# Kernel optimization log

Hardware: AMD Instinct MI355X
Metric: run time of the kernel (lower is better)

## Reference

```python
import jax, jax.numpy as jnp
import numpy as np

L_Q, B, Q = 512, 256, 512
IN, H, A = 512, 1024, 512
L_H = 512


def _xavier(key, shape):
    fan_out, fan_in = shape
    lim = (6.0 / (fan_in + fan_out)) ** 0.5
    return jax.random.uniform(key, shape, minval=-lim, maxval=lim, dtype=jnp.float32)


def setup_inputs() -> dict:
    key = jax.random.key(0)
    ks = jax.random.split(key, 12)
    return {
        "query_data": jax.random.normal(ks[0], (L_Q, B, Q), dtype=jnp.float32),
        "query_mask": jnp.ones((L_Q, B), dtype=jnp.float32),
        "input": jax.random.normal(ks[1], (B, IN), dtype=jnp.float32),
        "parent_index": jax.random.randint(ks[2], (B,), 0, L_H),
        "history": jax.random.normal(ks[3], (L_H, B, H), dtype=jnp.float32),
        "h0": jax.random.normal(ks[4], (B, H), dtype=jnp.float32),
        "c0": jax.random.normal(ks[5], (B, H), dtype=jnp.float32),
        "W_ih": _xavier(ks[6], (4 * H, IN + Q + H)),
        "W_hh": _xavier(ks[7], (4 * H, H)),
        "b_ih": jnp.zeros((4 * H,), dtype=jnp.float32),
        "b_hh": jnp.zeros((4 * H,), dtype=jnp.float32),
        "att1_w": _xavier(ks[8], (A, Q + H)),
        "att1_b": jnp.zeros((A,), dtype=jnp.float32),
        "att2_w": _xavier(ks[9], (1, A)),
        "att2_b": jnp.zeros((1,), dtype=jnp.float32),
    }


def reference(query_data, query_mask, input, parent_index, history, h0, c0,
              W_ih, W_hh, b_ih, b_hh, att1_w, att1_b, att2_w, att2_b):
    L_q, Bn, _ = query_data.shape
    # attention: concat broadcast h0 with query, two linears + tanh
    h_ctx = jnp.broadcast_to(h0[None], (L_q, Bn, h0.shape[1]))
    att = jnp.concatenate([h_ctx, query_data], axis=2)          # (L_q, B, H+Q)
    att_hidden = jnp.tanh(att @ att1_w.T + att1_b)               # (L_q, B, A)
    att_raw = (att_hidden @ att2_w.T + att2_b)[..., 0]           # (L_q, B)
    # manual masked softmax over L_q (faithful: max taken before masking)
    e = jnp.exp(att_raw - jnp.max(att_raw, axis=0, keepdims=True)) * query_mask
    w = e / jnp.sum(e, axis=0, keepdims=True)                    # (L_q, B)
    ctx_vec = jnp.sum(query_data * w[..., None], axis=0)         # (B, Q)
    # query_history: gather instead of one-hot matmul
    h_parent = history[parent_index, jnp.arange(Bn)]             # (B, H)
    # LSTMCell (dropout=0 -> identity); torch gate order i, f, g, o
    x = jnp.concatenate([input, ctx_vec, h_parent], axis=1)      # (B, IN+Q+H)
    gates = x @ W_ih.T + b_ih + h0 @ W_hh.T + b_hh               # (B, 4H)
    i, f, g, o = jnp.split(gates, 4, axis=1)
    c1 = jax.nn.sigmoid(f) * c0 + jax.nn.sigmoid(i) * jnp.tanh(g)
    h1 = jax.nn.sigmoid(o) * jnp.tanh(c1)
    return ctx_vec, h1, c1
```

## Files before the change

### kernel.cpp

```cpp
#include <hip/hip_runtime.h>
#include <hip/hip_bf16.h>


typedef short bf16x8 __attribute__((ext_vector_type(8)));
typedef float f32x4 __attribute__((ext_vector_type(4)));
typedef unsigned short u16x4 __attribute__((ext_vector_type(4)));

__device__ __forceinline__ unsigned short f2bf(float f) {
  unsigned int u = __builtin_bit_cast(unsigned int, f);
  u += 0x7fffu + ((u >> 16) & 1u);
  return (unsigned short)(u >> 16);
}
__device__ __forceinline__ float bf2f(unsigned short u) {
  unsigned int x = (unsigned int)u << 16;
  return __builtin_bit_cast(float, x);
}
__device__ __forceinline__ float fast_tanh(float x) {
  float e = __expf(2.0f * x);
  return 1.0f - 2.0f / (e + 1.0f);
}
__device__ __forceinline__ float fast_sig(float x) {
  return 1.0f / (1.0f + __expf(-x));
}
__device__ __forceinline__ f32x4 mfma16(bf16x8 a, bf16x8 b, f32x4 c) {
  return __builtin_amdgcn_mfma_f32_16x16x32_bf16(a, b, c, 0, 0, 0);
}

__global__ void k_prep(const float* __restrict__ a1w, const float* __restrict__ h0,
                       unsigned short* __restrict__ wqf, float* __restrict__ part1) {
  __shared__ float sh[4096], swt[4096];
  int bx = blockIdx.x;
  if (bx < 128) {
    int g = bx * 256 + threadIdx.x;
    int lane = g & 63, frag = g >> 6;
    int ab = frag >> 4, ksf = frag & 15;
    int a = ab * 16 + (lane & 15);
    int k = ksf * 32 + (lane >> 4) * 8;
    const float* src = a1w + (size_t)a * 1536 + 1024 + k;
    float4 v0 = *reinterpret_cast<const float4*>(src);
    float4 v1 = *reinterpret_cast<const float4*>(src + 4);
    unsigned short* dst = wqf + ((size_t)frag * 64 + lane) * 8;
    *(u16x4*)dst       = u16x4{ f2bf(v0.x), f2bf(v0.y), f2bf(v0.z), f2bf(v0.w) };
    *(u16x4*)(dst + 4) = u16x4{ f2bf(v1.x), f2bf(v1.y), f2bf(v1.z), f2bf(v1.w) };
    return;
  }
  int blk = bx - 128;
  int at = blk & 7, bt = (blk >> 3) & 3, ksp = blk >> 5;
  int a0 = at * 64, b0 = bt * 64, kbase = ksp * 128;
  int t = threadIdx.x;
  int ta = t & 15, tb = t >> 4;
  float acc[4][4] = {};
  for (int half = 0; half < 2; half++) {
    int k0 = kbase + half * 64;
    for (int i = 0; i < 4; i++) {
      int u = i * 256 + t;
      int row = u >> 4, c4 = (u & 15) << 2;
      float4 vh = *reinterpret_cast<const float4*>(h0 + (size_t)(b0 + row) * 1024 + k0 + c4);
      float4 vw = *reinterpret_cast<const float4*>(a1w + (size_t)(a0 + row) * 1536 + k0 + c4);
      int off = (row * 256 + c4 * 4) ^ ((row & 7) << 4);
      *(float4*)((char*)sh + off) = vh;
      *(float4*)((char*)swt + off) = vw;
    }
    __syncthreads();
    for (int k4 = 0; k4 < 16; k4++) {
      float4 hv[4], wv[4];
#pragma unroll
      for (int i = 0; i < 4; i++) {
        int rh = tb + 16 * i;
        hv[i] = *(const float4*)((char*)sh + ((rh * 256 + k4 * 16) ^ ((rh & 7) << 4)));
        int ra = ta + 16 * i;
        wv[i] = *(const float4*)((char*)swt + ((ra * 256 + k4 * 16) ^ ((ra & 7) << 4)));
      }
#pragma unroll
      for (int i = 0; i < 4; i++)
#pragma unroll
        for (int j = 0; j < 4; j++)
          acc[i][j] += hv[i].x * wv[j].x + hv[i].y * wv[j].y +
                       hv[i].z * wv[j].z + hv[i].w * wv[j].w;
    }
    __syncthreads();
  }
  float* dst = part1 + (size_t)ksp * 131072;
#pragma unroll
  for (int i = 0; i < 4; i++)
#pragma unroll
    for (int j = 0; j < 4; j++)
      dst[(size_t)(b0 + tb + 16 * i) * 512 + a0 + ta + 16 * j] = acc[i][j];
}

__global__ void k_base2(const float* __restrict__ part1, const float* __restrict__ a1b,
                        float* __restrict__ base) {
  int idx = blockIdx.x * 256 + threadIdx.x;
  float s = a1b[idx & 511];
  for (int ks = 0; ks < 8; ks++) s += part1[(size_t)ks * 131072 + idx];
  base[idx] = s;
}

__global__ __launch_bounds__(512, 2) void k_attgemm(
    const float* __restrict__ qd, const unsigned short* __restrict__ wqf,
    const float* __restrict__ base, const float* __restrict__ w2,
    const float* __restrict__ mask, float* __restrict__ nump,
    float* __restrict__ denp) {
  extern __shared__ char smem[];
  float* sRed = (float*)(smem + 131072);
  float* e_lds = (float*)(smem + 131072 + 2048);
  int t = threadIdx.x;
  int bt = blockIdx.x & 15, lt = blockIdx.x >> 4;
  int b0 = bt * 16, l0 = lt * 16;
  int lane = t & 63, lr = lane & 15, lh = lane >> 4;
  int w = t >> 6;
  int b_own = t >> 5, q0 = (t & 31) * 16;
  float ctx_acc[16] = {};
  float den_acc = 0.0f;

  for (int i = 0; i < 16; i++) {
    int u = i * 512 + t;
    int row = u >> 7, c4 = (u & 127) << 2;
    float4 v = *reinterpret_cast<const float4*>(
        qd + ((size_t)(l0 + (row >> 4)) * 256 + b0 + (row & 15)) * 512 + c4);
    int loff = (row * 1024 + c4 * 2) ^ ((row & 7) << 4);
    *(u16x4*)(smem + loff) = u16x4{ f2bf(v.x), f2bf(v.y), f2bf(v.z), f2bf(v.w) };
  }
  __syncthreads();

  for (int ls = 0; ls < 4; ls++) {
    char* cb = smem + (size_t)(ls & 1) * 65536;
    char* nb = smem + (size_t)((ls + 1) & 1) * 65536;
    int lb1 = l0 + (ls + 1) * 4;
    f32x4 acc[4][4] = {};
    float4 sv[4];
    for (int ks4 = 0; ks4 < 4; ks4++) {
      if (ls < 3) {
#pragma unroll
        for (int i = 0; i < 4; i++) {
          int u = (ks4 * 4 + i) * 512 + t;
          int row = u >> 7, c4 = (u & 127) << 2;
          sv[i] = *reinterpret_cast<const float4*>(
              qd + ((size_t)(lb1 + (row >> 4)) * 256 + b0 + (row & 15)) * 512 + c4);
        }
      }
#pragma unroll
      for (int ksl = 0; ksl < 4; ksl++) {
        int ks = ks4 * 4 + ksl;
        bf16x8 aF[4], bF[4];
#pragma unroll
        for (int mi = 0; mi < 4; mi++) {
          int row = mi * 16 + lr;
          int off = (row * 1024 + (ks * 32 + lh * 8) * 2) ^ ((row & 7) << 4);
          aF[mi] = *(const bf16x8*)(cb + off);
        }
#pragma unroll
        for (int ni = 0; ni < 4; ni++) {
          int ab = w * 4 + ni;
          bF[ni] = *(const bf16x8*)(wqf + ((size_t)(ab * 16 + ks) * 64 + lane) * 8);
        }
#pragma unroll
        for (int mi = 0; mi < 4; mi++)
#pragma unroll
          for (int ni = 0; ni < 4; ni++)
            acc[mi][ni] = mfma16(aF[mi], bF[ni], acc[mi][ni]);
      }
      if (ls < 3) {
#pragma unroll
        for (int i = 0; i < 4; i++) {
          int u = (ks4 * 4 + i) * 512 + t;
          int row = u >> 7, c4 = (u & 127) << 2;
          int loff = (row * 1024 + c4 * 2) ^ ((row & 7) << 4);
          *(u16x4*)(nb + loff) =
              u16x4{ f2bf(sv[i].x), f2bf(sv[i].y), f2bf(sv[i].z), f2bf(sv[i].w) };
        }
      }
    }
    float rs[4][4] = {};
#pragma unroll
    for (int ni = 0; ni < 4; ni++) {
      int a = w * 64 + ni * 16 + lr;
      float w2v = w2[a];
#pragma unroll
      for (int mi = 0; mi < 4; mi++)
#pragma unroll
        for (int r = 0; r < 4; r++) {
          int b = b0 + lh * 4 + r;
          float val = acc[mi][ni][r] + base[(size_t)b * 512 + a];
          rs[mi][r] += fast_tanh(val) * w2v;
        }
    }
#pragma unroll
    for (int mi = 0; mi < 4; mi++)
#pragma unroll
      for (int r = 0; r < 4; r++) {
        float v = rs[mi][r];
        v += __shfl_xor(v, 1); v += __shfl_xor(v, 2);
        v += __shfl_xor(v, 4); v += __shfl_xor(v, 8);
        rs[mi][r] = v;
      }
    if (lr == 0)
#pragma unroll
      for (int mi = 0; mi < 4; mi++)
#pragma unroll
        for (int r = 0; r < 4; r++)
          sRed[w * 64 + mi * 16 + lh * 4 + r] = rs[mi][r];
    __syncthreads();
    if (t < 64) {
      float araw = 0.0f;
#pragma unroll
      for (int j = 0; j < 8; j++) araw += sRed[j * 64 + t];
      int l = l0 + ls * 4 + (t >> 4), b = b0 + (t & 15);
      e_lds[t] = __expf(araw) * mask[(size_t)l * 256 + b];
    }
    __syncthreads();
#pragma unroll
    for (int li = 0; li < 4; li++) {
      int row = li * 16 + b_own;
      float e = e_lds[row];
      if ((t & 31) == 0) den_acc += e;
      int sw = (row & 7) << 4;
      bf16x8 v0 = *(const bf16x8*)(cb + ((row * 1024 + q0 * 2) ^ sw));
      bf16x8 v1 = *(const bf16x8*)(cb + ((row * 1024 + q0 * 2 + 16) ^ sw));
#pragma unroll
      for (int j = 0; j < 8; j++) {
        ctx_acc[j]     += e * bf2f((unsigned short)v0[j]);
        ctx_acc[8 + j] += e * bf2f((unsigned short)v1[j]);
      }
    }
    __syncthreads();
  }
  float* dst = nump + ((size_t)lt * 256 + b0 + b_own) * 512 + q0;
#pragma unroll
  for (int j = 0; j < 4; j++)
    *reinterpret_cast<float4*>(dst + j * 4) =
        float4{ ctx_acc[j * 4], ctx_acc[j * 4 + 1], ctx_acc[j * 4 + 2], ctx_acc[j * 4 + 3] };
  if ((t & 31) == 0) denp[lt * 256 + b0 + b_own] = den_acc;
}

__global__ void k_xf(const float* __restrict__ inp, const float* __restrict__ nump,
                     const float* __restrict__ denp, const float* __restrict__ hist,
                     const int* __restrict__ pidx, const float* __restrict__ h0,
                     unsigned short* __restrict__ xf, float* __restrict__ outF) {
  int g = blockIdx.x * 256 + threadIdx.x;
  int lane = g & 63, frag = g >> 6;
  int mb = frag / 96, kstep = frag % 96;
  int b = mb * 16 + (lane & 15);
  int k = kstep * 32 + (lane >> 4) * 8;
  float4 v0, v1;
  if (k >= 512 && k < 1024) {
    int q0 = k - 512;
    float d = 0.0f;
    v0 = float4{0, 0, 0, 0}; v1 = float4{0, 0, 0, 0};
#pragma unroll 4
    for (int lt = 0; lt < 32; lt++) {
      d += denp[lt * 256 + b];
      const float* p = nump + ((size_t)lt * 256 + b) * 512 + q0;
      float4 a0 = *reinterpret_cast<const float4*>(p);
      float4 a1 = *reinterpret_cast<const float4*>(p + 4);
      v0.x += a0.x; v0.y += a0.y; v0.z += a0.z; v0.w += a0.w;
      v1.x += a1.x; v1.y += a1.y; v1.z += a1.z; v1.w += a1.w;
    }
    float inv = 1.0f / d;
    v0.x *= inv; v0.y *= inv; v0.z *= inv; v0.w *= inv;
    v1.x *= inv; v1.y *= inv; v1.z *= inv; v1.w *= inv;
    *reinterpret_cast<float4*>(outF + (size_t)b * 512 + q0) = v0;
    *reinterpret_cast<float4*>(outF + (size_t)b * 512 + q0 + 4) = v1;
  } else {
    const float* src;
    if (k < 512)       src = inp  + (size_t)b * 512 + k;
    else if (k < 2048) src = hist + ((size_t)pidx[b] * 256 + b) * 1024 + (k - 1024);
    else               src = h0   + (size_t)b * 1024 + (k - 2048);
    v0 = *reinterpret_cast<const float4*>(src);
    v1 = *reinterpret_cast<const float4*>(src + 4);
  }
  unsigned short* dst = xf + ((size_t)frag * 64 + lane) * 8;
  *(u16x4*)dst       = u16x4{ f2bf(v0.x), f2bf(v0.y), f2bf(v0.z), f2bf(v0.w) };
  *(u16x4*)(dst + 4) = u16x4{ f2bf(v1.x), f2bf(v1.y), f2bf(v1.z), f2bf(v1.w) };
}

__global__ __launch_bounds__(256, 4) void k_gates(
    const unsigned short* __restrict__ xf, const float* __restrict__ Wih,
    const float* __restrict__ Whh, float* __restrict__ part) {
  int blk = blockIdx.x;
  int nt = blk & 127, ksp = blk >> 7;
  int n0 = nt * 32, kbeg = ksp * 768;
  int t = threadIdx.x;
  int lane = t & 63, lr = lane & 15, lh = lane >> 4;
  int w = t >> 6;
  f32x4 acc[4][2] = {};
#pragma unroll 2
  for (int ks = 0; ks < 24; ks++) {
    int k0 = kbeg + ks * 32;
    int kstep = k0 >> 5;
    bf16x8 aF[4], bF[2];
#pragma unroll
    for (int mi = 0; mi < 4; mi++) {
      int mb = w * 4 + mi;
      aF[mi] = *(const bf16x8*)(xf + ((size_t)(mb * 96 + kstep) * 64 + lane) * 8);
    }
    const float* Wp; int ldw, kk;
    if (k0 < 2048) { Wp = Wih; ldw = 2048; kk = k0; }
    else           { Wp = Whh; ldw = 1024; kk = k0 - 2048; }
#pragma unroll
    for (int ni = 0; ni < 2; ni++) {
      int j = n0 + ni * 16 + lr;
      const float* src = Wp + (size_t)j * ldw + kk + lh * 8;
      float4 v0 = *reinterpret_cast<const float4*>(src);
      float4 v1 = *reinterpret_cast<const float4*>(src + 4);
      bf16x8 bv;
      bv[0] = (short)f2bf(v0.x); bv[1] = (short)f2bf(v0.y);
      bv[2] = (short)f2bf(v0.z); bv[3] = (short)f2bf(v0.w);
      bv[4] = (short)f2bf(v1.x); bv[5] = (short)f2bf(v1.y);
      bv[6] = (short)f2bf(v1.z); bv[7] = (short)f2bf(v1.w);
      bF[ni] = bv;
    }
#pragma unroll
    for (int mi = 0; mi < 4; mi++)
#pragma unroll
      for (int ni = 0; ni < 2; ni++)
        acc[mi][ni] = mfma16(aF[mi], bF[ni], acc[mi][ni]);
  }
  float* dst = part + (size_t)ksp * (256 * 4096);
#pragma unroll
  for (int mi = 0; mi < 4; mi++)
#pragma unroll
    for (int ni = 0; ni < 2; ni++)
#pragma unroll
      for (int r = 0; r < 4; r++) {
        int b = w * 64 + mi * 16 + lh * 4 + r;
        int j = n0 + ni * 16 + lr;
        dst[(size_t)b * 4096 + j] = acc[mi][ni][r];
      }
}

__global__ void k_lstm(const float* __restrict__ part, const float* __restrict__ bih,
                       const float* __restrict__ bhh, const float* __restrict__ c0,
                       float* __restrict__ out) {
  int idx = blockIdx.x * 256 + threadIdx.x;
  int h = idx & 1023;
  int b = idx >> 10;
  const float* p = part + (size_t)b * 4096;
  float gi = bih[h] + bhh[h];
  float gf = bih[1024 + h] + bhh[1024 + h];
  float gg = bih[2048 + h] + bhh[2048 + h];
  float go = bih[3072 + h] + bhh[3072 + h];
#pragma unroll
  for (int ks = 0; ks < 4; ks++) {
    const float* q = p + (size_t)ks * 1048576;
    gi += q[h]; gf += q[1024 + h]; gg += q[2048 + h]; go += q[3072 + h];
  }
  float c = fast_sig(gf) * c0[idx] + fast_sig(gi) * fast_tanh(gg);
  float hv = fast_sig(go) * fast_tanh(c);
  out[131072 + idx] = hv;
  out[393216 + idx] = c;
}

extern "C" void kernel_launch(void* const* d_in, const int* in_sizes, int n_in,
                              void* d_out, int out_size, void* d_ws, size_t ws_size,
                              hipStream_t stream) {
  const float* qd    = (const float*)d_in[0];
  const float* qmask = (const float*)d_in[1];
  const float* inp   = (const float*)d_in[2];
  const int*   pidx  = (const int*)d_in[3];
  const float* hist  = (const float*)d_in[4];
  const float* h0    = (const float*)d_in[5];
  const float* c0    = (const float*)d_in[6];
  const float* Wih   = (const float*)d_in[7];
  const float* Whh   = (const float*)d_in[8];
  const float* bih   = (const float*)d_in[9];
  const float* bhh   = (const float*)d_in[10];
  const float* a1w   = (const float*)d_in[11];
  const float* a1b   = (const float*)d_in[12];
  const float* a2w   = (const float*)d_in[13];
  float* outF = (float*)d_out;

  char* ws = (char*)d_ws;
  unsigned short* wqf  = (unsigned short*)(ws);
  float*          base = (float*)(ws + 524288);
  float*          p1   = (float*)(ws + 1048576);
  unsigned short* xf   = (unsigned short*)(ws + 5242880);
  float*          denp = (float*)(ws + 6815744);
  float*          nump = (float*)(ws + 8388608);
  float*          pg   = (float*)(ws + 25165824);

  (void)hipFuncSetAttribute((const void*)k_attgemm,
                            hipFuncAttributeMaxDynamicSharedMemorySize, 133376);

  k_prep   <<<384,  256, 0, stream>>>(a1w, h0, wqf, p1);
  k_base2  <<<512,  256, 0, stream>>>(p1, a1b, base);
  k_attgemm<<<512,  512, 133376, stream>>>(qd, wqf, base, a2w, qmask, nump, denp);
  k_xf     <<<384,  256, 0, stream>>>(inp, nump, denp, hist, pidx, h0, xf, outF);
  k_gates  <<<512,  256, 0, stream>>>(xf, Wih, Whh, pg);
  k_lstm   <<<1024, 256, 0, stream>>>(pg, bih, bhh, c0, outF);
}
```

Baseline: 237.9 us.

## Halve attention GEMM block size and drop LDS double-buffering for occupancy

The attention-scoring kernel now runs 256-thread blocks with a single 64KB LDS buffer instead of 512 threads with a double-buffered 128KB tile. Each wave computes two A-chunks sequentially, and each thread accumulates 32 context columns instead of 16. The aim is to cut LDS use so more blocks fit per CU. In exchange, global loads of the next query tile no longer overlap with MFMA work, and each thread carries more accumulator registers.

```diff
diff --git a/kernel.cpp b/kernel.cpp
--- a/kernel.cpp
+++ b/kernel.cpp
@@ -96,62 +96,49 @@
   base[idx] = s;
 }
 
-__global__ __launch_bounds__(512, 2) void k_attgemm(
+__global__ __launch_bounds__(256, 2) void k_attgemm(
     const float* __restrict__ qd, const unsigned short* __restrict__ wqf,
     const float* __restrict__ base, const float* __restrict__ w2,
     const float* __restrict__ mask, float* __restrict__ nump,
     float* __restrict__ denp) {
   extern __shared__ char smem[];
-  float* sRed = (float*)(smem + 131072);
-  float* e_lds = (float*)(smem + 131072 + 2048);
+  float* sRed = (float*)(smem + 65536);
+  float* e_lds = (float*)(smem + 65536 + 1024);
   int t = threadIdx.x;
   int bt = blockIdx.x & 15, lt = blockIdx.x >> 4;
   int b0 = bt * 16, l0 = lt * 16;
   int lane = t & 63, lr = lane & 15, lh = lane >> 4;
   int w = t >> 6;
-  int b_own = t >> 5, q0 = (t & 31) * 16;
-  float ctx_acc[16] = {};
+  int b_own = t >> 4, qc = t & 15;
+  float ctx_acc[32] = {};
   float den_acc = 0.0f;
-
-  for (int i = 0; i < 16; i++) {
-    int u = i * 512 + t;
-    int row = u >> 7, c4 = (u & 127) << 2;
-    float4 v = *reinterpret_cast<const float4*>(
-        qd + ((size_t)(l0 + (row >> 4)) * 256 + b0 + (row & 15)) * 512 + c4);
-    int loff = (row * 1024 + c4 * 2) ^ ((row & 7) << 4);
-    *(u16x4*)(smem + loff) = u16x4{ f2bf(v.x), f2bf(v.y), f2bf(v.z), f2bf(v.w) };
-  }
-  __syncthreads();
-
   for (int ls = 0; ls < 4; ls++) {
-    char* cb = smem + (size_t)(ls & 1) * 65536;
-    char* nb = smem + (size_t)((ls + 1) & 1) * 65536;
-    int lb1 = l0 + (ls + 1) * 4;
-    f32x4 acc[4][4] = {};
-    float4 sv[4];
-    for (int ks4 = 0; ks4 < 4; ks4++) {
-      if (ls < 3) {
-#pragma unroll
-        for (int i = 0; i < 4; i++) {
-          int u = (ks4 * 4 + i) * 512 + t;
-          int row = u >> 7, c4 = (u & 127) << 2;
-          sv[i] = *reinterpret_cast<const float4*>(
-              qd + ((size_t)(lb1 + (row >> 4)) * 256 + b0 + (row & 15)) * 512 + c4);
-        }
-      }
-#pragma unroll
-      for (int ksl = 0; ksl < 4; ksl++) {
-        int ks = ks4 * 4 + ksl;
+    int l_base = l0 + ls * 4;
+    for (int i = 0; i < 32; i++) {
+      int u = i * 256 + t;
+      int row = u >> 7, c4 = (u & 127) << 2;
+      float4 v = *reinterpret_cast<const float4*>(
+          qd + ((size_t)(l_base + (row >> 4)) * 256 + b0 + (row & 15)) * 512 + c4);
+      int loff = (row * 1024 + c4 * 2) ^ ((row & 7) << 4);
+      *(u16x4*)(smem + loff) = u16x4{ f2bf(v.x), f2bf(v.y), f2bf(v.z), f2bf(v.w) };
+    }
+    __syncthreads();
+    float rs[4][4] = {};
+#pragma unroll
+    for (int chunk = 0; chunk < 2; chunk++) {
+      f32x4 acc[4][4] = {};
+#pragma unroll 4
+      for (int ks = 0; ks < 16; ks++) {
         bf16x8 aF[4], bF[4];
 #pragma unroll
         for (int mi = 0; mi < 4; mi++) {
           int row = mi * 16 + lr;
           int off = (row * 1024 + (ks * 32 + lh * 8) * 2) ^ ((row & 7) << 4);
-          aF[mi] = *(const bf16x8*)(cb + off);
+          aF[mi] = *(const bf16x8*)(smem + off);
         }
 #pragma unroll
         for (int ni = 0; ni < 4; ni++) {
-          int ab = w * 4 + ni;
+          int ab = chunk * 16 + w * 4 + ni;
           bF[ni] = *(const bf16x8*)(wqf + ((size_t)(ab * 16 + ks) * 64 + lane) * 8);
         }
 #pragma unroll
@@ -160,30 +147,19 @@
           for (int ni = 0; ni < 4; ni++)
             acc[mi][ni] = mfma16(aF[mi], bF[ni], acc[mi][ni]);
       }
-      if (ls < 3) {
-#pragma unroll
-        for (int i = 0; i < 4; i++) {
-          int u = (ks4 * 4 + i) * 512 + t;
-          int row = u >> 7, c4 = (u & 127) << 2;
-          int loff = (row * 1024 + c4 * 2) ^ ((row & 7) << 4);
-          *(u16x4*)(nb + loff) =
-              u16x4{ f2bf(sv[i].x), f2bf(sv[i].y), f2bf(sv[i].z), f2bf(sv[i].w) };
-        }
-      }
-    }
-    float rs[4][4] = {};
-#pragma unroll
-    for (int ni = 0; ni < 4; ni++) {
-      int a = w * 64 + ni * 16 + lr;
-      float w2v = w2[a];
-#pragma unroll
-      for (int mi = 0; mi < 4; mi++)
-#pragma unroll
-        for (int r = 0; r < 4; r++) {
-          int b = b0 + lh * 4 + r;
-          float val = acc[mi][ni][r] + base[(size_t)b * 512 + a];
-          rs[mi][r] += fast_tanh(val) * w2v;
-        }
+#pragma unroll
+      for (int ni = 0; ni < 4; ni++) {
+        int a = chunk * 256 + w * 64 + ni * 16 + lr;
+        float w2v = w2[a];
+#pragma unroll
+        for (int mi = 0; mi < 4; mi++)
+#pragma unroll
+          for (int r = 0; r < 4; r++) {
+            int b = b0 + lh * 4 + r;
+            float val = acc[mi][ni][r] + base[(size_t)b * 512 + a];
+            rs[mi][r] += fast_tanh(val) * w2v;
+          }
+      }
     }
 #pragma unroll
     for (int mi = 0; mi < 4; mi++)
@@ -202,10 +178,8 @@
           sRed[w * 64 + mi * 16 + lh * 4 + r] = rs[mi][r];
     __syncthreads();
     if (t < 64) {
-      float araw = 0.0f;
-#pragma unroll
-      for (int j = 0; j < 8; j++) araw += sRed[j * 64 + t];
-      int l = l0 + ls * 4 + (t >> 4), b = b0 + (t & 15);
+      float araw = sRed[t] + sRed[64 + t] + sRed[128 + t] + sRed[192 + t];
+      int l = l_base + (t >> 4), b = b0 + (t & 15);
       e_lds[t] = __expf(araw) * mask[(size_t)l * 256 + b];
     }
     __syncthreads();
@@ -213,24 +187,24 @@
     for (int li = 0; li < 4; li++) {
       int row = li * 16 + b_own;
       float e = e_lds[row];
-      if ((t & 31) == 0) den_acc += e;
+      if (qc == 0) den_acc += e;
       int sw = (row & 7) << 4;
-      bf16x8 v0 = *(const bf16x8*)(cb + ((row * 1024 + q0 * 2) ^ sw));
-      bf16x8 v1 = *(const bf16x8*)(cb + ((row * 1024 + q0 * 2 + 16) ^ sw));
-#pragma unroll
-      for (int j = 0; j < 8; j++) {
-        ctx_acc[j]     += e * bf2f((unsigned short)v0[j]);
-        ctx_acc[8 + j] += e * bf2f((unsigned short)v1[j]);
-      }
-    }
-    __syncthreads();
-  }
-  float* dst = nump + ((size_t)lt * 256 + b0 + b_own) * 512 + q0;
-#pragma unroll
-  for (int j = 0; j < 4; j++)
+#pragma unroll
+      for (int j = 0; j < 4; j++) {
+        bf16x8 v = *(const bf16x8*)(smem + ((row * 1024 + qc * 64 + j * 16) ^ sw));
+#pragma unroll
+        for (int x = 0; x < 8; x++)
+          ctx_acc[j * 8 + x] += e * bf2f((unsigned short)v[x]);
+      }
+    }
+    __syncthreads();
+  }
+  float* dst = nump + ((size_t)lt * 256 + b0 + b_own) * 512 + qc * 32;
+#pragma unroll
+  for (int j = 0; j < 8; j++)
     *reinterpret_cast<float4*>(dst + j * 4) =
         float4{ ctx_acc[j * 4], ctx_acc[j * 4 + 1], ctx_acc[j * 4 + 2], ctx_acc[j * 4 + 3] };
-  if ((t & 31) == 0) denp[lt * 256 + b0 + b_own] = den_acc;
+  if (qc == 0) denp[lt * 256 + b0 + b_own] = den_acc;
 }
 
 __global__ void k_xf(const float* __restrict__ inp, const float* __restrict__ nump,
@@ -380,11 +354,11 @@
   float*          pg   = (float*)(ws + 25165824);
 
   (void)hipFuncSetAttribute((const void*)k_attgemm,
-                            hipFuncAttributeMaxDynamicSharedMemorySize, 133376);
+                            hipFuncAttributeMaxDynamicSharedMemorySize, 66816);
 
   k_prep   <<<384,  256, 0, stream>>>(a1w, h0, wqf, p1);
   k_base2  <<<512,  256, 0, stream>>>(p1, a1b, base);
-  k_attgemm<<<512,  512, 133376, stream>>>(qd, wqf, base, a2w, qmask, nump, denp);
+  k_attgemm<<<512,  256, 66816, stream>>>(qd, wqf, base, a2w, qmask, nump, denp);
   k_xf     <<<384,  256, 0, stream>>>(inp, nump, denp, hist, pidx, h0, xf, outF);
   k_gates  <<<512,  256, 0, stream>>>(xf, Wih, Whh, pg);
   k_lstm   <<<1024, 256, 0, stream>>>(pg, bih, bhh, c0, outF);
```

New measurement: 299.3 us. 25.8% more time.
